# Optimization experiments

Measured on AMD Instinct MI355X. Metric: run time of the kernel, lower is better.

## Reference

```python
import jax, jax.numpy as jnp
import numpy as np

B, S, D = 2, 2048, 768
H = 12
HD = D // H  # 64
SCALE = HD ** -0.5


def setup_inputs() -> dict:
    key = jax.random.key(0)
    k1, k2, k3, k4, k5 = jax.random.split(key, 5)
    x = jax.random.normal(k1, (B, S, D), dtype=jnp.float32)
    w_qkv = jax.random.normal(k2, (D, 3 * D), dtype=jnp.float32) * (D ** -0.5)
    b_qkv = jax.random.normal(k3, (3 * D,), dtype=jnp.float32) * 0.02
    w_proj = jax.random.normal(k4, (D, D), dtype=jnp.float32) * (D ** -0.5)
    b_proj = jax.random.normal(k5, (D,), dtype=jnp.float32) * 0.02
    return {"x": x, "w_qkv": w_qkv, "b_qkv": b_qkv, "w_proj": w_proj, "b_proj": b_proj}


def reference(x, w_qkv, b_qkv, w_proj, b_proj):
    b, s, d = x.shape
    # QKV projection: (B,S,3D) -> (3,B,H,S,HD)
    qkv = x @ w_qkv + b_qkv
    qkv = qkv.reshape(b, s, 3, H, HD).transpose(2, 0, 3, 1, 4)
    q, k, v = qkv[0], qkv[1], qkv[2]
    q = q * SCALE
    # full NxN attention scores, as in the original module
    attn = jnp.einsum("bhqd,bhkd->bhqk", q, k)
    attn = jax.nn.softmax(attn, axis=-1)
    out = jnp.einsum("bhqk,bhkd->bhqd", attn, v)  # (B,H,S,HD)
    out = out.transpose(0, 2, 1, 3).reshape(b, s, d)
    return out @ w_proj + b_proj
```

## Files before the change

kernel.cpp:

```cpp
#include <hip/hip_runtime.h>
#include <hip/hip_bf16.h>

#define B_ 2
#define S_ 2048
#define D_ 768
#define H_ 12
#define HD_ 64
#define EXP2C_ 0.1803368801111244f

typedef __attribute__((ext_vector_type(8))) short bf16x8;
typedef __attribute__((ext_vector_type(8))) unsigned short u16x8;
typedef __attribute__((ext_vector_type(4))) float f32x4;
typedef __attribute__((ext_vector_type(4))) unsigned int u32x4;

static __device__ __forceinline__ unsigned short f2bf(float x) {
    union { float f; unsigned u; } v; v.f = x;
    unsigned r = (v.u + 0x7FFFu + ((v.u >> 16) & 1u)) >> 16;
    return (unsigned short)r;
}
static __device__ __forceinline__ float bf2f(unsigned short h) {
    union { unsigned u; float f; } v; v.u = ((unsigned)h) << 16;
    return v.f;
}
static __device__ __forceinline__ float fexp2(float x) { return __builtin_exp2f(x); }

static __device__ __forceinline__ unsigned pk_bf16(float a, float b) {
    __hip_bfloat162 pk = __float22bfloat162_rn(make_float2(a, b));
    union { __hip_bfloat162 h; unsigned u; } v; v.h = pk;
    return v.u;
}

static __device__ __forceinline__ f32x4 mfma32(bf16x8 a, bf16x8 b, f32x4 c) {
    return __builtin_amdgcn_mfma_f32_16x16x32_bf16(a, b, c, 0, 0, 0);
}

typedef __attribute__((address_space(3))) unsigned int lds_u32;
typedef __attribute__((address_space(1))) const unsigned int glb_u32;
static __device__ __forceinline__ void glds16(const unsigned short* g, unsigned short* l) {
    __builtin_amdgcn_global_load_lds((glb_u32*)g, (lds_u32*)l, 16, 0, 0);
}

#define PREP_CONV_ 1536
#define PREP_TQKV_ 1728
#define PREP_TPRJ_ 576
__global__ __launch_bounds__(256) void prep_kernel(
    const float* __restrict__ x,      unsigned short* __restrict__ x16,
    const float* __restrict__ w_qkv,  unsigned short* __restrict__ wqkvT,
    const float* __restrict__ w_proj, unsigned short* __restrict__ wprojT)
{
    __shared__ float tile[32][33];
    const int bid = blockIdx.x, t = threadIdx.x;
    if (bid < PREP_CONV_) {
        const int i = (bid * 256 + t) * 8;
        float4 a0 = *(const float4*)(x + i);
        float4 a1 = *(const float4*)(x + i + 4);
        u16x8 s;
        s[0] = f2bf(a0.x); s[1] = f2bf(a0.y); s[2] = f2bf(a0.z); s[3] = f2bf(a0.w);
        s[4] = f2bf(a1.x); s[5] = f2bf(a1.y); s[6] = f2bf(a1.z); s[7] = f2bf(a1.w);
        *(u16x8*)(x16 + i) = s;
        return;
    }
    const float* w; unsigned short* wT; int N, bb;
    if (bid < PREP_CONV_ + PREP_TQKV_) { w = w_qkv; wT = wqkvT; N = 3 * D_; bb = bid - PREP_CONV_; }
    else                               { w = w_proj; wT = wprojT; N = D_;   bb = bid - PREP_CONV_ - PREP_TQKV_; }
    const int K = D_;
    const int nt = N / 32;
    const int n0 = (bb % nt) * 32, k0 = (bb / nt) * 32;
    const int tx = t & 31, ty = t >> 5;
#pragma unroll
    for (int i = 0; i < 4; i++)
        tile[ty + i * 8][tx] = w[(size_t)(k0 + ty + i * 8) * N + n0 + tx];
    __syncthreads();
#pragma unroll
    for (int i = 0; i < 4; i++)
        wT[(size_t)(n0 + ty + i * 8) * K + k0 + tx] = f2bf(tile[tx][ty + i * 8]);
}

template <int BM, int BN, bool OUT_F32>
__global__ __launch_bounds__(256) void gemm_bt_kernel(
    const unsigned short* __restrict__ A,
    const unsigned short* __restrict__ Bt,
    const float* __restrict__ bias,
    void* __restrict__ Cp,
    int M, int N, int K)
{
    __shared__ __align__(16) unsigned short As[BM][32];
    __shared__ __align__(16) unsigned short Bs[BN][32];
    constexpr int MI = BM / 32, NJ = BN / 32;
    constexpr int ACH = BM * 4, BCH = BN * 4;

    const int t = threadIdx.x;
    const int w = t >> 6, lane = t & 63, quad = lane >> 4, l16 = lane & 15;
    const int n0 = blockIdx.x * BN, m0 = blockIdx.y * BM;
    const int mw = (w & 1) * (BM / 2), nw = (w >> 1) * (BN / 2);

    const f32x4 z = {0.f, 0.f, 0.f, 0.f};
    f32x4 acc[MI][NJ];
#pragma unroll
    for (int i = 0; i < MI; i++)
#pragma unroll
        for (int j = 0; j < NJ; j++) acc[i][j] = z;

    for (int kk = 0; kk < K; kk += 32) {
#pragma unroll
        for (int it = 0; it < (ACH + 255) / 256; it++) {
            const int c = t + it * 256;
            if (ACH % 256 == 0 || c < ACH) {
                const int row = c >> 2, c8 = (c & 3) << 3;
                glds16(A + (size_t)(m0 + row) * K + kk + c8, &As[0][0] + c * 8);
            }
        }
#pragma unroll
        for (int it = 0; it < (BCH + 255) / 256; it++) {
            const int c = t + it * 256;
            if (BCH % 256 == 0 || c < BCH) {
                const int row = c >> 2, c8 = (c & 3) << 3;
                glds16(Bt + (size_t)(n0 + row) * K + kk + c8, &Bs[0][0] + c * 8);
            }
        }
        __syncthreads();

        bf16x8 a[MI], b[NJ];
#pragma unroll
        for (int i = 0; i < MI; i++)
            a[i] = *(const bf16x8*)(&As[mw + i * 16 + l16][quad * 8]);
#pragma unroll
        for (int j = 0; j < NJ; j++)
            b[j] = *(const bf16x8*)(&Bs[nw + j * 16 + l16][quad * 8]);
#pragma unroll
        for (int i = 0; i < MI; i++)
#pragma unroll
            for (int j = 0; j < NJ; j++)
                acc[i][j] = mfma32(a[i], b[j], acc[i][j]);
        __syncthreads();
    }

#pragma unroll
    for (int j = 0; j < NJ; j++) {
        const int col = n0 + nw + j * 16 + l16;
        const float bv = bias[col];
#pragma unroll
        for (int i = 0; i < MI; i++) {
#pragma unroll
            for (int r = 0; r < 4; r++) {
                const int row = m0 + mw + i * 16 + quad * 4 + r;
                const float v = acc[i][j][r] + bv;
                if (OUT_F32) ((float*)Cp)[(size_t)row * N + col] = v;
                else         ((unsigned short*)Cp)[(size_t)row * N + col] = f2bf(v);
            }
        }
    }
}

__global__ __launch_bounds__(256) void repack_v_kernel(
    const unsigned short* __restrict__ qkv,
    unsigned short* __restrict__ vt)
{
    __shared__ unsigned short T[64][65];
    const int t = threadIdx.x;
    const int bh = blockIdx.x, st = blockIdx.y;
    const int b = bh / H_, h = bh % H_;
    const unsigned short* src =
        qkv + (size_t)(b * S_ + st * 64) * (3 * D_) + 2 * D_ + h * HD_;

#pragma unroll
    for (int it = 0; it < 2; it++) {
        const int c = t + it * 256, sr = c >> 3, g = c & 7;
        u16x8 v = *(const u16x8*)(src + (size_t)sr * (3 * D_) + g * 8);
#pragma unroll
        for (int j = 0; j < 8; j++) T[sr][g * 8 + j] = v[j];
    }
    __syncthreads();
#pragma unroll
    for (int it = 0; it < 2; it++) {
        const int c = t + it * 256, hd = c >> 3, g = c & 7;
        u16x8 v;
#pragma unroll
        for (int j = 0; j < 8; j++) v[j] = T[g * 8 + j][hd];
        *(u16x8*)(vt + (size_t)(bh * HD_ + hd) * S_ + st * 64 + g * 8) = v;
    }
}

__global__ __launch_bounds__(256) void attn_kernel(
    const unsigned short* __restrict__ qkv,
    const unsigned short* __restrict__ vt,
    unsigned short* __restrict__ o)
{
    __shared__ __align__(16) unsigned short Ks[2][64][64];
    __shared__ __align__(16) unsigned short Vs[2][64][64];

    const int t = threadIdx.x;
    const int w = t >> 6, lane = t & 63, quad = lane >> 4, l16 = lane & 15;
    const int h8 = l16 & 7;
    const int qt = blockIdx.x, bh = blockIdx.y;
    const int b = bh / H_, h = bh % H_;
    const int ld = 3 * D_;

    const unsigned short* qbase =
        qkv + (size_t)(b * S_ + qt * 64 + 16 * w + l16) * ld + h * HD_;
    u16x8 qr0 = *(const u16x8*)(qbase + quad * 8);
    u16x8 qr1 = *(const u16x8*)(qbase + 32 + quad * 8);
    bf16x8 qf0, qf1;
#pragma unroll
    for (int j = 0; j < 8; j++) {
        qf0[j] = (short)f2bf(bf2f(qr0[j]) * EXP2C_);
        qf1[j] = (short)f2bf(bf2f(qr1[j]) * EXP2C_);
    }

    const unsigned short* kbase = qkv + (size_t)(b * S_) * ld + D_ + h * HD_;
    const unsigned short* vbase = vt + (size_t)bh * HD_ * S_;

    const f32x4 z = {0.f, 0.f, 0.f, 0.f};
    f32x4 o_acc[4] = {z, z, z, z};
    f32x4 l4[4] = {z, z, z, z};

#pragma unroll
    for (int it = 0; it < 2; it++) {
        const int c = t + it * 256, row = c >> 3, g = c & 7;
        const int sgK = g ^ ((row & 3) | (((row >> 3) & 1) << 2));
        const int sgV = g ^ (row & 7);
        *(u16x8*)(&Ks[0][row][sgK * 8]) = *(const u16x8*)(kbase + (size_t)row * ld + g * 8);
        *(u16x8*)(&Vs[0][row][sgV * 8]) = *(const u16x8*)(vbase + (size_t)row * S_ + g * 8);
    }
    __syncthreads();

    const int NT = S_ / 64;
    for (int kt = 0; kt < NT; kt++) {
        const int buf = kt & 1;
        const bool pre = (kt + 1 < NT);

        u16x8 pk[2], pv[2];
        if (pre) {
            const int kr1 = (kt + 1) * 64;
#pragma unroll
            for (int i = 0; i < 2; i++) {
                const int c = t + i * 256, row = c >> 3, g = c & 7;
                pk[i] = *(const u16x8*)(kbase + (size_t)(kr1 + row) * ld + g * 8);
                pv[i] = *(const u16x8*)(vbase + (size_t)row * S_ + kr1 + g * 8);
            }
        }

        f32x4 s_acc[4] = {z, z, z, z};
#pragma unroll
        for (int nt = 0; nt < 4; nt++) {
            const int rowp = ((nt >> 1) << 5) + ((l16 >> 2) << 3) + ((nt & 1) << 2) + (l16 & 3);
            const int skr = (rowp & 3) | (((rowp >> 3) & 1) << 2);
            const unsigned short* kr = &Ks[buf][rowp][0];
            bf16x8 k0 = *(const bf16x8*)(kr + (quad ^ skr) * 8);
            bf16x8 k1 = *(const bf16x8*)(kr + ((quad ^ skr) ^ 4) * 8);
            s_acc[nt] = mfma32(k0, qf0, s_acc[nt]);
            s_acc[nt] = mfma32(k1, qf1, s_acc[nt]);
        }

        f32x4 pr[4];
#pragma unroll
        for (int nt = 0; nt < 4; nt++) {
#pragma unroll
            for (int r = 0; r < 4; r++) pr[nt][r] = fexp2(s_acc[nt][r]);
            l4[nt] += pr[nt];
        }
        union { u32x4 u; bf16x8 h; } ca, cb;
        ca.u[0] = pk_bf16(pr[0][0], pr[0][1]);
        ca.u[1] = pk_bf16(pr[0][2], pr[0][3]);
        ca.u[2] = pk_bf16(pr[1][0], pr[1][1]);
        ca.u[3] = pk_bf16(pr[1][2], pr[1][3]);
        cb.u[0] = pk_bf16(pr[2][0], pr[2][1]);
        cb.u[1] = pk_bf16(pr[2][2], pr[2][3]);
        cb.u[2] = pk_bf16(pr[3][0], pr[3][1]);
        cb.u[3] = pk_bf16(pr[3][2], pr[3][3]);
        const bf16x8 pa0 = ca.h, pa1 = cb.h;

#pragma unroll
        for (int nt = 0; nt < 4; nt++) {
            const int row = nt * 16 + l16;
            bf16x8 v0 = *(const bf16x8*)(&Vs[buf][row][(quad ^ h8) * 8]);
            bf16x8 v1 = *(const bf16x8*)(&Vs[buf][row][((quad + 4) ^ h8) * 8]);
            o_acc[nt] = mfma32(pa0, v0, o_acc[nt]);
            o_acc[nt] = mfma32(pa1, v1, o_acc[nt]);
        }

        if (pre) {
#pragma unroll
            for (int i = 0; i < 2; i++) {
                const int c = t + i * 256, row = c >> 3, g = c & 7;
                const int sgK = g ^ ((row & 3) | (((row >> 3) & 1) << 2));
                const int sgV = g ^ (row & 7);
                *(u16x8*)(&Ks[buf ^ 1][row][sgK * 8]) = pk[i];
                *(u16x8*)(&Vs[buf ^ 1][row][sgV * 8]) = pv[i];
            }
        }
        __syncthreads();
    }

    float l = 0.f;
#pragma unroll
    for (int nt = 0; nt < 4; nt++)
        l += l4[nt][0] + l4[nt][1] + l4[nt][2] + l4[nt][3];
    l += __shfl_xor(l, 16, 64);
    l += __shfl_xor(l, 32, 64);
#pragma unroll
    for (int r = 0; r < 4; r++) {
        const float lr = __shfl(l, quad * 4 + r, 64);
        const float inv = 1.f / lr;
        const int row = b * S_ + qt * 64 + 16 * w + quad * 4 + r;
        unsigned short* ob = o + (size_t)row * D_ + h * HD_;
#pragma unroll
        for (int nt = 0; nt < 4; nt++)
            ob[nt * 16 + l16] = f2bf(o_acc[nt][r] * inv);
    }
}

extern "C" void kernel_launch(void* const* d_in, const int* in_sizes, int n_in,
                              void* d_out, int out_size, void* d_ws, size_t ws_size,
                              hipStream_t stream) {
    const float* x      = (const float*)d_in[0];
    const float* w_qkv  = (const float*)d_in[1];
    const float* b_qkv  = (const float*)d_in[2];
    const float* w_proj = (const float*)d_in[3];
    const float* b_proj = (const float*)d_in[4];
    float* out = (float*)d_out;

    unsigned short* qkv    = (unsigned short*)d_ws;
    unsigned short* vtb    = qkv    + (size_t)(B_ * S_) * (3 * D_);
    unsigned short* o_x16  = vtb    + (size_t)(B_ * H_) * HD_ * S_;
    unsigned short* wqkvT  = o_x16  + (size_t)(B_ * S_) * D_;
    unsigned short* wprojT = wqkvT  + (size_t)D_ * (3 * D_);

    dim3 blk(256);
    prep_kernel<<<dim3(PREP_CONV_ + PREP_TQKV_ + PREP_TPRJ_), blk, 0, stream>>>(
        x, o_x16, w_qkv, wqkvT, w_proj, wprojT);
    gemm_bt_kernel<128, 96, false><<<dim3((3 * D_) / 96, (B_ * S_) / 128), blk, 0, stream>>>(
        o_x16, wqkvT, b_qkv, qkv, B_ * S_, 3 * D_, D_);
    repack_v_kernel<<<dim3(B_ * H_, S_ / 64), blk, 0, stream>>>(qkv, vtb);
    attn_kernel<<<dim3(S_ / 64, B_ * H_), blk, 0, stream>>>(qkv, vtb, o_x16);
    gemm_bt_kernel<64, 64, true><<<dim3(D_ / 64, (B_ * S_) / 64), blk, 0, stream>>>(
        o_x16, wprojT, b_proj, out, B_ * S_, D_, D_);
}
```

Baseline: 173.5 us.

## Give each attention wave two 16-row query tiles and compute row sums via MFMA

The attention block shrinks from 4 to 2 waves, and each wave now handles 32 query rows as two 16-row tiles. This reuses every K and V fragment read from shared memory across two MFMA sets, halving LDS reads per unit of work. Softmax row sums are now accumulated with an MFMA against a ones vector, replacing the VALU adds and cross-lane shuffles. The cost is higher register pressure and fewer waves per block to hide latency. The row sum is now taken from bf16-rounded probabilities, which slightly changes numerics.

```diff
diff --git a/kernel.cpp b/kernel.cpp
--- a/kernel.cpp
+++ b/kernel.cpp
@@ -181,7 +181,7 @@
     }
 }
 
-__global__ __launch_bounds__(256) void attn_kernel(
+__global__ __launch_bounds__(128) void attn_kernel(
     const unsigned short* __restrict__ qkv,
     const unsigned short* __restrict__ vt,
     unsigned short* __restrict__ o)
@@ -196,27 +196,35 @@
     const int b = bh / H_, h = bh % H_;
     const int ld = 3 * D_;
 
-    const unsigned short* qbase =
-        qkv + (size_t)(b * S_ + qt * 64 + 16 * w + l16) * ld + h * HD_;
-    u16x8 qr0 = *(const u16x8*)(qbase + quad * 8);
-    u16x8 qr1 = *(const u16x8*)(qbase + 32 + quad * 8);
-    bf16x8 qf0, qf1;
+    const unsigned short* qb0 =
+        qkv + (size_t)(b * S_ + qt * 64 + w * 32 + l16) * ld + h * HD_;
+    u16x8 qr00 = *(const u16x8*)(qb0 + quad * 8);
+    u16x8 qr01 = *(const u16x8*)(qb0 + 32 + quad * 8);
+    u16x8 qr10 = *(const u16x8*)(qb0 + (size_t)16 * ld + quad * 8);
+    u16x8 qr11 = *(const u16x8*)(qb0 + (size_t)16 * ld + 32 + quad * 8);
+    bf16x8 qf00, qf01, qf10, qf11;
 #pragma unroll
     for (int j = 0; j < 8; j++) {
-        qf0[j] = (short)f2bf(bf2f(qr0[j]) * EXP2C_);
-        qf1[j] = (short)f2bf(bf2f(qr1[j]) * EXP2C_);
-    }
+        qf00[j] = (short)f2bf(bf2f(qr00[j]) * EXP2C_);
+        qf01[j] = (short)f2bf(bf2f(qr01[j]) * EXP2C_);
+        qf10[j] = (short)f2bf(bf2f(qr10[j]) * EXP2C_);
+        qf11[j] = (short)f2bf(bf2f(qr11[j]) * EXP2C_);
+    }
+
+    bf16x8 ones;
+#pragma unroll
+    for (int j = 0; j < 8; j++) ones[j] = (short)0x3F80;
 
     const unsigned short* kbase = qkv + (size_t)(b * S_) * ld + D_ + h * HD_;
     const unsigned short* vbase = vt + (size_t)bh * HD_ * S_;
 
     const f32x4 z = {0.f, 0.f, 0.f, 0.f};
-    f32x4 o_acc[4] = {z, z, z, z};
-    f32x4 l4[4] = {z, z, z, z};
-
-#pragma unroll
-    for (int it = 0; it < 2; it++) {
-        const int c = t + it * 256, row = c >> 3, g = c & 7;
+    f32x4 o0[4] = {z, z, z, z}, o1[4] = {z, z, z, z};
+    f32x4 l0 = z, l1 = z;
+
+#pragma unroll
+    for (int i = 0; i < 4; i++) {
+        const int c = t + i * 128, row = c >> 3, g = c & 7;
         const int sgK = g ^ ((row & 3) | (((row >> 3) & 1) << 2));
         const int sgV = g ^ (row & 7);
         *(u16x8*)(&Ks[0][row][sgK * 8]) = *(const u16x8*)(kbase + (size_t)row * ld + g * 8);
@@ -229,18 +237,20 @@
         const int buf = kt & 1;
         const bool pre = (kt + 1 < NT);
 
-        u16x8 pk[2], pv[2];
+        u16x8 pk[4], pv[4];
         if (pre) {
             const int kr1 = (kt + 1) * 64;
 #pragma unroll
-            for (int i = 0; i < 2; i++) {
-                const int c = t + i * 256, row = c >> 3, g = c & 7;
+            for (int i = 0; i < 4; i++) {
+                const int c = t + i * 128, row = c >> 3, g = c & 7;
                 pk[i] = *(const u16x8*)(kbase + (size_t)(kr1 + row) * ld + g * 8);
                 pv[i] = *(const u16x8*)(vbase + (size_t)row * S_ + kr1 + g * 8);
             }
         }
 
-        f32x4 s_acc[4] = {z, z, z, z};
+        f32x4 s0[4], s1[4];
+#pragma unroll
+        for (int nt = 0; nt < 4; nt++) { s0[nt] = z; s1[nt] = z; }
 #pragma unroll
         for (int nt = 0; nt < 4; nt++) {
             const int rowp = ((nt >> 1) << 5) + ((l16 >> 2) << 3) + ((nt & 1) << 2) + (l16 & 3);
@@ -248,41 +258,65 @@
             const unsigned short* kr = &Ks[buf][rowp][0];
             bf16x8 k0 = *(const bf16x8*)(kr + (quad ^ skr) * 8);
             bf16x8 k1 = *(const bf16x8*)(kr + ((quad ^ skr) ^ 4) * 8);
-            s_acc[nt] = mfma32(k0, qf0, s_acc[nt]);
-            s_acc[nt] = mfma32(k1, qf1, s_acc[nt]);
-        }
-
-        f32x4 pr[4];
-#pragma unroll
-        for (int nt = 0; nt < 4; nt++) {
-#pragma unroll
-            for (int r = 0; r < 4; r++) pr[nt][r] = fexp2(s_acc[nt][r]);
-            l4[nt] += pr[nt];
-        }
-        union { u32x4 u; bf16x8 h; } ca, cb;
-        ca.u[0] = pk_bf16(pr[0][0], pr[0][1]);
-        ca.u[1] = pk_bf16(pr[0][2], pr[0][3]);
-        ca.u[2] = pk_bf16(pr[1][0], pr[1][1]);
-        ca.u[3] = pk_bf16(pr[1][2], pr[1][3]);
-        cb.u[0] = pk_bf16(pr[2][0], pr[2][1]);
-        cb.u[1] = pk_bf16(pr[2][2], pr[2][3]);
-        cb.u[2] = pk_bf16(pr[3][0], pr[3][1]);
-        cb.u[3] = pk_bf16(pr[3][2], pr[3][3]);
-        const bf16x8 pa0 = ca.h, pa1 = cb.h;
-
+            s0[nt] = mfma32(k0, qf00, s0[nt]);
+            s0[nt] = mfma32(k1, qf01, s0[nt]);
+            s1[nt] = mfma32(k0, qf10, s1[nt]);
+            s1[nt] = mfma32(k1, qf11, s1[nt]);
+        }
+
+        bf16x8 vr0[4], vr1[4];
 #pragma unroll
         for (int nt = 0; nt < 4; nt++) {
             const int row = nt * 16 + l16;
-            bf16x8 v0 = *(const bf16x8*)(&Vs[buf][row][(quad ^ h8) * 8]);
-            bf16x8 v1 = *(const bf16x8*)(&Vs[buf][row][((quad + 4) ^ h8) * 8]);
-            o_acc[nt] = mfma32(pa0, v0, o_acc[nt]);
-            o_acc[nt] = mfma32(pa1, v1, o_acc[nt]);
+            vr0[nt] = *(const bf16x8*)(&Vs[buf][row][(quad ^ h8) * 8]);
+            vr1[nt] = *(const bf16x8*)(&Vs[buf][row][((quad ^ h8) ^ 4) * 8]);
+        }
+
+        f32x4 p0[4], p1[4];
+#pragma unroll
+        for (int nt = 0; nt < 4; nt++) {
+#pragma unroll
+            for (int r = 0; r < 4; r++) {
+                p0[nt][r] = fexp2(s0[nt][r]);
+                p1[nt][r] = fexp2(s1[nt][r]);
+            }
+        }
+        union { u32x4 u; bf16x8 h; } a00, a01, a10, a11;
+        a00.u[0] = pk_bf16(p0[0][0], p0[0][1]);
+        a00.u[1] = pk_bf16(p0[0][2], p0[0][3]);
+        a00.u[2] = pk_bf16(p0[1][0], p0[1][1]);
+        a00.u[3] = pk_bf16(p0[1][2], p0[1][3]);
+        a01.u[0] = pk_bf16(p0[2][0], p0[2][1]);
+        a01.u[1] = pk_bf16(p0[2][2], p0[2][3]);
+        a01.u[2] = pk_bf16(p0[3][0], p0[3][1]);
+        a01.u[3] = pk_bf16(p0[3][2], p0[3][3]);
+        a10.u[0] = pk_bf16(p1[0][0], p1[0][1]);
+        a10.u[1] = pk_bf16(p1[0][2], p1[0][3]);
+        a10.u[2] = pk_bf16(p1[1][0], p1[1][1]);
+        a10.u[3] = pk_bf16(p1[1][2], p1[1][3]);
+        a11.u[0] = pk_bf16(p1[2][0], p1[2][1]);
+        a11.u[1] = pk_bf16(p1[2][2], p1[2][3]);
+        a11.u[2] = pk_bf16(p1[3][0], p1[3][1]);
+        a11.u[3] = pk_bf16(p1[3][2], p1[3][3]);
+        const bf16x8 pa00 = a00.h, pa01 = a01.h, pa10 = a10.h, pa11 = a11.h;
+
+        l0 = mfma32(pa00, ones, l0);
+        l0 = mfma32(pa01, ones, l0);
+        l1 = mfma32(pa10, ones, l1);
+        l1 = mfma32(pa11, ones, l1);
+
+#pragma unroll
+        for (int nt = 0; nt < 4; nt++) {
+            o0[nt] = mfma32(pa00, vr0[nt], o0[nt]);
+            o0[nt] = mfma32(pa01, vr1[nt], o0[nt]);
+            o1[nt] = mfma32(pa10, vr0[nt], o1[nt]);
+            o1[nt] = mfma32(pa11, vr1[nt], o1[nt]);
         }
 
         if (pre) {
 #pragma unroll
-            for (int i = 0; i < 2; i++) {
-                const int c = t + i * 256, row = c >> 3, g = c & 7;
+            for (int i = 0; i < 4; i++) {
+                const int c = t + i * 128, row = c >> 3, g = c & 7;
                 const int sgK = g ^ ((row & 3) | (((row >> 3) & 1) << 2));
                 const int sgV = g ^ (row & 7);
                 *(u16x8*)(&Ks[buf ^ 1][row][sgK * 8]) = pk[i];
@@ -292,21 +326,18 @@
         __syncthreads();
     }
 
-    float l = 0.f;
-#pragma unroll
-    for (int nt = 0; nt < 4; nt++)
-        l += l4[nt][0] + l4[nt][1] + l4[nt][2] + l4[nt][3];
-    l += __shfl_xor(l, 16, 64);
-    l += __shfl_xor(l, 32, 64);
 #pragma unroll
     for (int r = 0; r < 4; r++) {
-        const float lr = __shfl(l, quad * 4 + r, 64);
-        const float inv = 1.f / lr;
-        const int row = b * S_ + qt * 64 + 16 * w + quad * 4 + r;
-        unsigned short* ob = o + (size_t)row * D_ + h * HD_;
-#pragma unroll
-        for (int nt = 0; nt < 4; nt++)
-            ob[nt * 16 + l16] = f2bf(o_acc[nt][r] * inv);
+        const float i0 = 1.f / l0[r];
+        const float i1 = 1.f / l1[r];
+        const int row0 = b * S_ + qt * 64 + w * 32 + quad * 4 + r;
+        unsigned short* ob0 = o + (size_t)row0 * D_ + h * HD_;
+        unsigned short* ob1 = ob0 + (size_t)16 * D_;
+#pragma unroll
+        for (int nt = 0; nt < 4; nt++) {
+            ob0[nt * 16 + l16] = f2bf(o0[nt][r] * i0);
+            ob1[nt * 16 + l16] = f2bf(o1[nt][r] * i1);
+        }
     }
 }
 
@@ -332,7 +363,7 @@
     gemm_bt_kernel<128, 96, false><<<dim3((3 * D_) / 96, (B_ * S_) / 128), blk, 0, stream>>>(
         o_x16, wqkvT, b_qkv, qkv, B_ * S_, 3 * D_, D_);
     repack_v_kernel<<<dim3(B_ * H_, S_ / 64), blk, 0, stream>>>(qkv, vtb);
-    attn_kernel<<<dim3(S_ / 64, B_ * H_), blk, 0, stream>>>(qkv, vtb, o_x16);
+    attn_kernel<<<dim3(S_ / 64, B_ * H_), dim3(128), 0, stream>>>(qkv, vtb, o_x16);
     gemm_bt_kernel<64, 64, true><<<dim3(D_ / 64, (B_ * S_) / 64), blk, 0, stream>>>(
         o_x16, wprojT, b_proj, out, B_ * S_, D_, D_);
 }
```

New measurement: 180.2 us. 1.04x slower.

## Use direct global-to-LDS loads and MFMA row sums in attention loop

Applied to the files above, without the earlier changes.

Replaces the register-staged K/V prefetch with direct global-to-LDS async loads (glds16), pre-swizzling the source addresses so the LDS layout stays the same. This drops the register round trip and the separate LDS store phase. The softmax denominator is now computed with an MFMA against a vector of ones instead of per-element adds plus cross-lane shuffles. V fragments are also loaded from LDS before the exp step so the reads overlap with it. The risks are correctness of the swizzle mapping with the direct-load layout, and the extra MFMA work for the row sums.

```diff
diff --git a/kernel.cpp b/kernel.cpp
--- a/kernel.cpp
+++ b/kernel.cpp
@@ -207,37 +207,48 @@
         qf1[j] = (short)f2bf(bf2f(qr1[j]) * EXP2C_);
     }
 
+    bf16x8 ones;
+#pragma unroll
+    for (int j = 0; j < 8; j++) ones[j] = (short)0x3F80;
+
     const unsigned short* kbase = qkv + (size_t)(b * S_) * ld + D_ + h * HD_;
     const unsigned short* vbase = vt + (size_t)bh * HD_ * S_;
 
+    const int c0 = t, c1 = t + 256;
+    const int row0 = c0 >> 3, row1 = c1 >> 3;
+    const int kg0 = (c0 & 7) ^ ((row0 & 3) | (((row0 >> 3) & 1) << 2));
+    const int kg1 = (c1 & 7) ^ ((row1 & 3) | (((row1 >> 3) & 1) << 2));
+    const int vg0 = (c0 & 7) ^ (row0 & 7);
+    const int vg1 = (c1 & 7) ^ (row1 & 7);
+    const unsigned short* kp0 = kbase + (size_t)row0 * ld + kg0 * 8;
+    const unsigned short* kp1 = kbase + (size_t)row1 * ld + kg1 * 8;
+    const unsigned short* vp0 = vbase + (size_t)row0 * S_ + vg0 * 8;
+    const unsigned short* vp1 = vbase + (size_t)row1 * S_ + vg1 * 8;
+    const size_t KSTEP = (size_t)64 * ld;
+
     const f32x4 z = {0.f, 0.f, 0.f, 0.f};
     f32x4 o_acc[4] = {z, z, z, z};
-    f32x4 l4[4] = {z, z, z, z};
-
-#pragma unroll
-    for (int it = 0; it < 2; it++) {
-        const int c = t + it * 256, row = c >> 3, g = c & 7;
-        const int sgK = g ^ ((row & 3) | (((row >> 3) & 1) << 2));
-        const int sgV = g ^ (row & 7);
-        *(u16x8*)(&Ks[0][row][sgK * 8]) = *(const u16x8*)(kbase + (size_t)row * ld + g * 8);
-        *(u16x8*)(&Vs[0][row][sgV * 8]) = *(const u16x8*)(vbase + (size_t)row * S_ + g * 8);
-    }
+    f32x4 l_acc = z;
+
+    glds16(kp0, &Ks[0][0][0] + c0 * 8);
+    glds16(kp1, &Ks[0][0][0] + c1 * 8);
+    glds16(vp0, &Vs[0][0][0] + c0 * 8);
+    glds16(vp1, &Vs[0][0][0] + c1 * 8);
+    kp0 += KSTEP; kp1 += KSTEP; vp0 += 64; vp1 += 64;
     __syncthreads();
 
     const int NT = S_ / 64;
     for (int kt = 0; kt < NT; kt++) {
         const int buf = kt & 1;
-        const bool pre = (kt + 1 < NT);
-
-        u16x8 pk[2], pv[2];
-        if (pre) {
-            const int kr1 = (kt + 1) * 64;
-#pragma unroll
-            for (int i = 0; i < 2; i++) {
-                const int c = t + i * 256, row = c >> 3, g = c & 7;
-                pk[i] = *(const u16x8*)(kbase + (size_t)(kr1 + row) * ld + g * 8);
-                pv[i] = *(const u16x8*)(vbase + (size_t)row * S_ + kr1 + g * 8);
-            }
+
+        if (kt + 1 < NT) {
+            unsigned short* kd = &Ks[buf ^ 1][0][0];
+            unsigned short* vd = &Vs[buf ^ 1][0][0];
+            glds16(kp0, kd + c0 * 8);
+            glds16(kp1, kd + c1 * 8);
+            glds16(vp0, vd + c0 * 8);
+            glds16(vp1, vd + c1 * 8);
+            kp0 += KSTEP; kp1 += KSTEP; vp0 += 64; vp1 += 64;
         }
 
         f32x4 s_acc[4] = {z, z, z, z};
@@ -252,12 +263,19 @@
             s_acc[nt] = mfma32(k1, qf1, s_acc[nt]);
         }
 
+        bf16x8 vr0[4], vr1[4];
+#pragma unroll
+        for (int nt = 0; nt < 4; nt++) {
+            const int row = nt * 16 + l16;
+            vr0[nt] = *(const bf16x8*)(&Vs[buf][row][(quad ^ h8) * 8]);
+            vr1[nt] = *(const bf16x8*)(&Vs[buf][row][((quad ^ h8) ^ 4) * 8]);
+        }
+
         f32x4 pr[4];
 #pragma unroll
         for (int nt = 0; nt < 4; nt++) {
 #pragma unroll
             for (int r = 0; r < 4; r++) pr[nt][r] = fexp2(s_acc[nt][r]);
-            l4[nt] += pr[nt];
         }
         union { u32x4 u; bf16x8 h; } ca, cb;
         ca.u[0] = pk_bf16(pr[0][0], pr[0][1]);
@@ -270,38 +288,21 @@
         cb.u[3] = pk_bf16(pr[3][2], pr[3][3]);
         const bf16x8 pa0 = ca.h, pa1 = cb.h;
 
+        l_acc = mfma32(pa0, ones, l_acc);
+        l_acc = mfma32(pa1, ones, l_acc);
+
 #pragma unroll
         for (int nt = 0; nt < 4; nt++) {
-            const int row = nt * 16 + l16;
-            bf16x8 v0 = *(const bf16x8*)(&Vs[buf][row][(quad ^ h8) * 8]);
-            bf16x8 v1 = *(const bf16x8*)(&Vs[buf][row][((quad + 4) ^ h8) * 8]);
-            o_acc[nt] = mfma32(pa0, v0, o_acc[nt]);
-            o_acc[nt] = mfma32(pa1, v1, o_acc[nt]);
-        }
-
-        if (pre) {
-#pragma unroll
-            for (int i = 0; i < 2; i++) {
-                const int c = t + i * 256, row = c >> 3, g = c & 7;
-                const int sgK = g ^ ((row & 3) | (((row >> 3) & 1) << 2));
-                const int sgV = g ^ (row & 7);
-                *(u16x8*)(&Ks[buf ^ 1][row][sgK * 8]) = pk[i];
-                *(u16x8*)(&Vs[buf ^ 1][row][sgV * 8]) = pv[i];
-            }
-        }
+            o_acc[nt] = mfma32(pa0, vr0[nt], o_acc[nt]);
+            o_acc[nt] = mfma32(pa1, vr1[nt], o_acc[nt]);
+        }
+
         __syncthreads();
     }
 
-    float l = 0.f;
-#pragma unroll
-    for (int nt = 0; nt < 4; nt++)
-        l += l4[nt][0] + l4[nt][1] + l4[nt][2] + l4[nt][3];
-    l += __shfl_xor(l, 16, 64);
-    l += __shfl_xor(l, 32, 64);
 #pragma unroll
     for (int r = 0; r < 4; r++) {
-        const float lr = __shfl(l, quad * 4 + r, 64);
-        const float inv = 1.f / lr;
+        const float inv = 1.f / l_acc[r];
         const int row = b * S_ + qt * 64 + 16 * w + quad * 4 + r;
         unsigned short* ob = o + (size_t)row * D_ + h * HD_;
 #pragma unroll
```

New measurement: 174.2 us. Within noise of the previous version (+0.4%).
